# Optimization experiments

Hardware: AMD Instinct MI355X
Metric: run time of the kernel (lower is better)

## Reference

```python
import jax, jax.numpy as jnp
import numpy as np

N_NODES = 50000
N_EDGES = 800000
IN_CH = 128
HID = 64
OUT_CH = 2
N_GRAPHS = 512


def gcn_conv(x, edge_index, W, b, num_nodes):
    # PyG GCNConv: h = x @ W, add self-loops, sym-normalize, scatter-add, add bias
    loop = jnp.arange(num_nodes, dtype=edge_index.dtype)
    src = jnp.concatenate([edge_index[0], loop])
    dst = jnp.concatenate([edge_index[1], loop])
    deg = jax.ops.segment_sum(jnp.ones_like(dst, dtype=x.dtype), dst, num_segments=num_nodes)
    dinv = jnp.where(deg > 0, jax.lax.rsqrt(deg), 0.0)
    norm = dinv[src] * dinv[dst]                      # [E+N]
    h = x @ W                                         # [N, HID]
    msg = h[src] * norm[:, None]                      # gather + scale
    out = jax.ops.segment_sum(msg, dst, num_segments=num_nodes)  # scatter-add
    return out + b


def global_mean_pool(x, batch, num_graphs):
    s = jax.ops.segment_sum(x, batch, num_segments=num_graphs)
    cnt = jax.ops.segment_sum(jnp.ones((x.shape[0],), x.dtype), batch, num_segments=num_graphs)
    return s / jnp.maximum(cnt, 1.0)[:, None]


def setup_inputs() -> dict:
    key = jax.random.key(0)
    ks = jax.random.split(key, 9)
    x = jax.random.normal(ks[0], (N_NODES, IN_CH), dtype=jnp.float32)
    edge_index = jax.random.randint(ks[1], (2, N_EDGES), 0, N_NODES, dtype=jnp.int64)
    batch = jnp.sort(jax.random.randint(ks[2], (N_NODES,), 0, N_GRAPHS, dtype=jnp.int64))
    W1 = jax.random.normal(ks[3], (IN_CH, HID), dtype=jnp.float32) * (1.0 / np.sqrt(IN_CH))
    b1 = jnp.zeros((HID,), dtype=jnp.float32)
    W2 = jax.random.normal(ks[4], (HID, HID), dtype=jnp.float32) * (1.0 / np.sqrt(HID))
    b2 = jnp.zeros((HID,), dtype=jnp.float32)
    Wl = jax.random.normal(ks[5], (HID, OUT_CH), dtype=jnp.float32) * (1.0 / np.sqrt(HID))
    bl = jnp.zeros((OUT_CH,), dtype=jnp.float32)
    return {"x": x, "edge_index": edge_index, "batch": batch,
            "W1": W1, "b1": b1, "W2": W2, "b2": b2, "Wl": Wl, "bl": bl}


def reference(x, edge_index, batch, W1, b1, W2, b2, Wl, bl):
    h = jax.nn.relu(gcn_conv(x, edge_index, W1, b1, N_NODES))
    h = jax.nn.relu(gcn_conv(h, edge_index, W2, b2, N_NODES))
    g = global_mean_pool(h, batch, N_GRAPHS)          # [N_GRAPHS, HID]
    return g @ Wl + bl                                # [N_GRAPHS, OUT_CH]
```

## Files before the change

### kernel.cpp

```cpp
#include <hip/hip_runtime.h>

constexpr int HID = 64;
constexpr int RB = 128;
constexpr int KC = 32;
constexpr int NPB = 128;
constexpr int MAXBUCK = 512;
constexpr int CAP = 2560;
constexpr int CHUNK = 4096;

__global__ __launch_bounds__(256) void k_bucket(const int* __restrict__ src,
                                                const int* __restrict__ dst, int nE,
                                                int* __restrict__ bcursor,
                                                int2* __restrict__ pairs, int nBuck) {
  __shared__ int hist[MAXBUCK];
  __shared__ int base[MAXBUCK];
  const int t = threadIdx.x;
  const int e0 = blockIdx.x * CHUNK;
  const int eEnd = min(e0 + CHUNK, nE);
  for (int i = t; i < nBuck; i += 256) hist[i] = 0;
  __syncthreads();
  for (int e = e0 + t; e < eEnd; e += 256)
    atomicAdd(&hist[dst[e] >> 7], 1);
  __syncthreads();
  for (int i = t; i < nBuck; i += 256) {
    int c = hist[i];
    int r = (c > 0) ? atomicAdd(&bcursor[i], c) : 0;
    base[i] = i * CAP + r;
    hist[i] = 0;
  }
  __syncthreads();
  for (int e = e0 + t; e < eEnd; e += 256) {
    int d = dst[e];
    int b = d >> 7;
    int idx = atomicAdd(&hist[b], 1);
    pairs[base[b] + idx] = make_int2(src[e], d);
  }
}

__global__ __launch_bounds__(256) void k_place(const int2* __restrict__ pairs,
                                               const int* __restrict__ bcursor,
                                               int* __restrict__ csr,
                                               int* __restrict__ row_lo,
                                               int* __restrict__ row_hi,
                                               float* __restrict__ dinv, int nN) {
  __shared__ int cnt[NPB], sc[NPB], cur[NPB];
  const int t = threadIdx.x;
  const int b = blockIdx.x;
  const int vbase = b * NPB;
  const int lo = b * CAP;
  const int npairs = bcursor[b];
  if (t < NPB) cnt[t] = 0;
  __syncthreads();
  for (int p = t; p < npairs; p += 256)
    atomicAdd(&cnt[pairs[lo + p].y - vbase], 1);
  __syncthreads();
  if (t < NPB) sc[t] = cnt[t];
  __syncthreads();
  for (int d = 1; d < NPB; d <<= 1) {
    int x = 0;
    if (t < NPB) { x = sc[t]; if (t >= d) x += sc[t - d]; }
    __syncthreads();
    if (t < NPB) sc[t] = x;
    __syncthreads();
  }
  if (t < NPB && vbase + t < nN) {
    int ex = sc[t] - cnt[t];
    row_lo[vbase + t] = lo + ex;
    row_hi[vbase + t] = lo + sc[t];
    dinv[vbase + t] = rsqrtf((float)cnt[t] + 1.0f);
    cur[t] = lo + ex;
  }
  __syncthreads();
  for (int p = t; p < npairs; p += 256) {
    int2 e = pairs[lo + p];
    int pos = atomicAdd(&cur[e.y - vbase], 1);
    csr[pos] = e.x;
  }
}

template <int K>
__global__ __launch_bounds__(256) void k_mm_tile(const float* __restrict__ X,
                                                 const float* __restrict__ W,
                                                 const float* __restrict__ dinv,
                                                 float* __restrict__ out, int nRows) {
  __shared__ float Xs[RB][KC + 1];
  __shared__ float Ws[KC][HID];

  const int t    = threadIdx.x;
  const int lane = t & 63;
  const int wid  = t >> 6;
  const int rg   = lane >> 3;
  const int cg   = lane & 7;
  const int rb   = blockIdx.x * RB;
  const int rloc = wid * 32 + rg * 4;

  float acc[4][8];
#pragma unroll
  for (int i = 0; i < 4; ++i)
#pragma unroll
    for (int j = 0; j < 8; ++j) acc[i][j] = 0.f;

  for (int c = 0; c < K / KC; ++c) {
    const int k0 = c * KC;
    {
      const int r  = t >> 1;
      const int kh = (t & 1) * 16;
      const int grow = rb + r;
      if (grow < nRows) {
        const float* p = X + (size_t)grow * K + k0 + kh;
#pragma unroll
        for (int q = 0; q < 4; ++q) {
          const float4 v = *(const float4*)(p + q * 4);
          float* d = &Xs[r][kh + q * 4];
          d[0] = v.x; d[1] = v.y; d[2] = v.z; d[3] = v.w;
        }
      }
    }
    {
      const float* p = W + (size_t)(k0 + (t >> 3)) * HID + (t & 7) * 8;
      const float4 v0 = *(const float4*)p;
      const float4 v1 = *(const float4*)(p + 4);
      float* d = &Ws[t >> 3][(t & 7) * 8];
      ((float4*)d)[0] = v0;
      ((float4*)d)[1] = v1;
    }
    __syncthreads();

#pragma unroll
    for (int k = 0; k < KC; ++k) {
      const float4 w0 = *(const float4*)&Ws[k][cg * 8];
      const float4 w1 = *(const float4*)&Ws[k][cg * 8 + 4];
      float xv[4];
#pragma unroll
      for (int i = 0; i < 4; ++i) xv[i] = Xs[rloc + i][k];
#pragma unroll
      for (int i = 0; i < 4; ++i) {
        acc[i][0] = fmaf(xv[i], w0.x, acc[i][0]);
        acc[i][1] = fmaf(xv[i], w0.y, acc[i][1]);
        acc[i][2] = fmaf(xv[i], w0.z, acc[i][2]);
        acc[i][3] = fmaf(xv[i], w0.w, acc[i][3]);
        acc[i][4] = fmaf(xv[i], w1.x, acc[i][4]);
        acc[i][5] = fmaf(xv[i], w1.y, acc[i][5]);
        acc[i][6] = fmaf(xv[i], w1.z, acc[i][6]);
        acc[i][7] = fmaf(xv[i], w1.w, acc[i][7]);
      }
    }
    __syncthreads();
  }

#pragma unroll
  for (int i = 0; i < 4; ++i) {
    const int row = rb + rloc + i;
    if (row < nRows) {
      const float s = dinv[row];
      float4 o0, o1;
      o0.x = acc[i][0] * s; o0.y = acc[i][1] * s; o0.z = acc[i][2] * s; o0.w = acc[i][3] * s;
      o1.x = acc[i][4] * s; o1.y = acc[i][5] * s; o1.z = acc[i][6] * s; o1.w = acc[i][7] * s;
      float* p = out + (size_t)row * HID + cg * 8;
      ((float4*)p)[0] = o0;
      ((float4*)p)[1] = o1;
    }
  }
}

__global__ __launch_bounds__(256) void k_gather4(const int* __restrict__ csr,
                                                 const int* __restrict__ row_lo,
                                                 const int* __restrict__ row_hi,
                                                 const float4* __restrict__ H4,
                                                 const float* __restrict__ dinv,
                                                 const float* __restrict__ b,
                                                 float4* __restrict__ out4, int nN) {
  const int t = threadIdx.x;
  const int wid = t >> 6;
  const int lane = t & 63;
  const int ng = lane >> 4;
  const int cq = lane & 15;
  const int v = blockIdx.x * 16 + wid * 4 + ng;
  const int vv = min(v, nN - 1);
  const int lo = row_lo[vv];
  const int cnt = row_hi[vv] - lo;

  double acc[4][4];
#pragma unroll
  for (int c = 0; c < 4; ++c)
#pragma unroll
    for (int q = 0; q < 4; ++q) acc[c][q] = 0.0;
  {
    const float4 sv = H4[(size_t)vv * 16 + cq];
    acc[0][0] = (double)sv.x; acc[0][1] = (double)sv.y;
    acc[0][2] = (double)sv.z; acc[0][3] = (double)sv.w;
  }

  for (int base = 0; base < cnt; base += 16) {
    int idxv = (base + cq < cnt) ? csr[lo + base + cq] : 0;
#pragma unroll
    for (int j = 0; j < 16; ++j) {
      int s = __shfl(idxv, (ng << 4) + j, 64);
      if (base + j < cnt) {
        const float4 h = H4[(size_t)s * 16 + cq];
        acc[j & 3][0] += (double)h.x;
        acc[j & 3][1] += (double)h.y;
        acc[j & 3][2] += (double)h.z;
        acc[j & 3][3] += (double)h.w;
      }
    }
  }

  if (v < nN) {
    const float dv = dinv[v];
    const float4 bb = ((const float4*)b)[cq];
    float4 o;
    o.x = fmaxf(fmaf(dv, (float)((acc[0][0] + acc[1][0]) + (acc[2][0] + acc[3][0])), bb.x), 0.f);
    o.y = fmaxf(fmaf(dv, (float)((acc[0][1] + acc[1][1]) + (acc[2][1] + acc[3][1])), bb.y), 0.f);
    o.z = fmaxf(fmaf(dv, (float)((acc[0][2] + acc[1][2]) + (acc[2][2] + acc[3][2])), bb.z), 0.f);
    o.w = fmaxf(fmaf(dv, (float)((acc[0][3] + acc[1][3]) + (acc[2][3] + acc[3][3])), bb.w), 0.f);
    out4[(size_t)v * 16 + cq] = o;
  }
}

__device__ inline int lowerb(const int* __restrict__ a, int n, int key) {
  int lo = 0, hi = n;
  while (lo < hi) {
    int mid = (lo + hi) >> 1;
    if (a[mid] < key) lo = mid + 1; else hi = mid;
  }
  return lo;
}

__global__ __launch_bounds__(256) void k_pool_head(const float* __restrict__ Z,
                                                   const int* __restrict__ batch, int nN,
                                                   const float* __restrict__ Wl,
                                                   const float* __restrict__ bl,
                                                   float* __restrict__ out) {
  int g = blockIdx.x;
  int lane = threadIdx.x & 63;
  int wid = threadIdx.x >> 6;
  int lo = lowerb(batch, nN, g);
  int hi = lowerb(batch, nN, g + 1);
  double acc = 0.0;
  for (int r = lo + wid; r < hi; r += 4) acc += (double)Z[(size_t)r * HID + lane];
  __shared__ double s[4][HID];
  s[wid][lane] = acc;
  __syncthreads();
  if (wid == 0) {
    double tot = (s[0][lane] + s[1][lane]) + (s[2][lane] + s[3][lane]);
    double mean = tot / (double)max(hi - lo, 1);
    double p0 = mean * (double)Wl[lane * 2 + 0];
    double p1 = mean * (double)Wl[lane * 2 + 1];
#pragma unroll
    for (int off = 32; off; off >>= 1) {
      p0 += __shfl_xor(p0, off, 64);
      p1 += __shfl_xor(p1, off, 64);
    }
    if (lane == 0) {
      out[g * 2 + 0] = (float)(p0 + (double)bl[0]);
      out[g * 2 + 1] = (float)(p1 + (double)bl[1]);
    }
  }
}

extern "C" void kernel_launch(void* const* d_in, const int* in_sizes, int n_in,
                              void* d_out, int out_size, void* d_ws, size_t ws_size,
                              hipStream_t stream) {
  const float* x     = (const float*)d_in[0];
  const int*   ei    = (const int*)d_in[1];
  const int*   batch = (const int*)d_in[2];
  const float* W1    = (const float*)d_in[3];
  const float* b1    = (const float*)d_in[4];
  const float* W2    = (const float*)d_in[5];
  const float* b2    = (const float*)d_in[6];
  const float* Wl    = (const float*)d_in[7];
  const float* bl    = (const float*)d_in[8];
  float* out = (float*)d_out;

  const int nN = in_sizes[2];
  const int nE = in_sizes[1] / 2;
  const int nG = out_size / 2;
  const int* src = ei;
  const int* dst = ei + nE;

  char* ws = (char*)d_ws;
  size_t off = 0;
  auto alloc = [&](size_t bytes) {
    char* p = ws + off;
    off += (bytes + 255) & ~(size_t)255;
    return p;
  };
  int*   bcursor = (int*)alloc(MAXBUCK * 4);
  int*   row_lo  = (int*)alloc((size_t)nN * 4);
  int*   row_hi  = (int*)alloc((size_t)nN * 4);
  int*   csr     = (int*)alloc((size_t)MAXBUCK * CAP * 4);
  float* dinv    = (float*)alloc((size_t)nN * 4);
  float* A       = (float*)alloc((size_t)nN * HID * 4);
  float* B       = (float*)alloc((size_t)nN * HID * 4);
  int2*  pairs   = (int2*)A;

  const int nBuck = (nN + NPB - 1) / NPB;

  hipMemsetAsync(bcursor, 0, MAXBUCK * 4, stream);
  k_bucket<<<(nE + CHUNK - 1) / CHUNK, 256, 0, stream>>>(src, dst, nE, bcursor, pairs, nBuck);
  k_place<<<nBuck, 256, 0, stream>>>(pairs, bcursor, csr, row_lo, row_hi, dinv, nN);

  k_mm_tile<128><<<(nN + RB - 1) / RB, 256, 0, stream>>>(x, W1, dinv, A, nN);
  k_gather4<<<(nN + 15) / 16, 256, 0, stream>>>(csr, row_lo, row_hi, (const float4*)A,
                                                dinv, b1, (float4*)B, nN);

  k_mm_tile<64><<<(nN + RB - 1) / RB, 256, 0, stream>>>(B, W2, dinv, A, nN);
  k_gather4<<<(nN + 15) / 16, 256, 0, stream>>>(csr, row_lo, row_hi, (const float4*)A,
                                                dinv, b2, (float4*)B, nN);

  k_pool_head<<<nG, 256, 0, stream>>>(B, batch, nN, Wl, bl, out);
}
```

Before: 149.9 us.

## Fuse layer-1 gather with layer-2 matmul into one kernel

```diff
diff --git a/kernel.cpp b/kernel.cpp
--- a/kernel.cpp
+++ b/kernel.cpp
@@ -6,7 +6,7 @@
 constexpr int NPB = 128;
 constexpr int MAXBUCK = 512;
 constexpr int CAP = 2560;
-constexpr int CHUNK = 4096;
+constexpr int CHUNK = 2048;
 
 __global__ __launch_bounds__(256) void k_bucket(const int* __restrict__ src,
                                                 const int* __restrict__ dst, int nE,
@@ -160,6 +160,89 @@
       ((float4*)p)[0] = o0;
       ((float4*)p)[1] = o1;
     }
+  }
+}
+
+__global__ __launch_bounds__(256) void k_gather_mm(const int* __restrict__ csr,
+                                                   const int* __restrict__ row_lo,
+                                                   const int* __restrict__ row_hi,
+                                                   const float4* __restrict__ H4,
+                                                   const float* __restrict__ dinv,
+                                                   const float* __restrict__ b,
+                                                   const float* __restrict__ W2,
+                                                   float4* __restrict__ out4, int nN) {
+  __shared__ float W2s[HID][HID];
+  __shared__ float z1s[16][68];
+
+  const int t = threadIdx.x;
+  for (int i = t; i < HID * HID / 4; i += 256)
+    ((float4*)W2s)[i] = ((const float4*)W2)[i];
+  __syncthreads();
+
+  const int wid = t >> 6;
+  const int lane = t & 63;
+  const int ng = lane >> 4;
+  const int cq = lane & 15;
+  const int nl = wid * 4 + ng;
+  const int v = blockIdx.x * 16 + nl;
+  const int vv = min(v, nN - 1);
+  const int lo = row_lo[vv];
+  const int cnt = row_hi[vv] - lo;
+
+  double acc[4][4];
+#pragma unroll
+  for (int c = 0; c < 4; ++c)
+#pragma unroll
+    for (int q = 0; q < 4; ++q) acc[c][q] = 0.0;
+  {
+    const float4 sv = H4[(size_t)vv * 16 + cq];
+    acc[0][0] = (double)sv.x; acc[0][1] = (double)sv.y;
+    acc[0][2] = (double)sv.z; acc[0][3] = (double)sv.w;
+  }
+
+  for (int base = 0; base < cnt; base += 16) {
+    int idxv = (base + cq < cnt) ? csr[lo + base + cq] : 0;
+#pragma unroll
+    for (int j = 0; j < 16; ++j) {
+      int s = __shfl(idxv, (ng << 4) + j, 64);
+      if (base + j < cnt) {
+        const float4 h = H4[(size_t)s * 16 + cq];
+        acc[j & 3][0] += (double)h.x;
+        acc[j & 3][1] += (double)h.y;
+        acc[j & 3][2] += (double)h.z;
+        acc[j & 3][3] += (double)h.w;
+      }
+    }
+  }
+
+  {
+    const float dv = dinv[vv];
+    const float4 bb = ((const float4*)b)[cq];
+    float4 z;
+    z.x = fmaxf(fmaf(dv, (float)((acc[0][0] + acc[1][0]) + (acc[2][0] + acc[3][0])), bb.x), 0.f);
+    z.y = fmaxf(fmaf(dv, (float)((acc[0][1] + acc[1][1]) + (acc[2][1] + acc[3][1])), bb.y), 0.f);
+    z.z = fmaxf(fmaf(dv, (float)((acc[0][2] + acc[1][2]) + (acc[2][2] + acc[3][2])), bb.z), 0.f);
+    z.w = fmaxf(fmaf(dv, (float)((acc[0][3] + acc[1][3]) + (acc[2][3] + acc[3][3])), bb.w), 0.f);
+    float* zp = &z1s[nl][cq * 4];
+    zp[0] = z.x; zp[1] = z.y; zp[2] = z.z; zp[3] = z.w;
+  }
+
+  float h0 = 0.f, h1 = 0.f, h2 = 0.f, h3 = 0.f;
+#pragma unroll 8
+  for (int k = 0; k < HID; ++k) {
+    const float zk = z1s[nl][k];
+    const float4 w = *(const float4*)&W2s[k][cq * 4];
+    h0 = fmaf(zk, w.x, h0);
+    h1 = fmaf(zk, w.y, h1);
+    h2 = fmaf(zk, w.z, h2);
+    h3 = fmaf(zk, w.w, h3);
+  }
+
+  if (v < nN) {
+    const float dv = dinv[v];
+    float4 o;
+    o.x = h0 * dv; o.y = h1 * dv; o.z = h2 * dv; o.w = h3 * dv;
+    out4[(size_t)v * 16 + cq] = o;
   }
 }
 
@@ -302,12 +385,12 @@
   k_place<<<nBuck, 256, 0, stream>>>(pairs, bcursor, csr, row_lo, row_hi, dinv, nN);
 
   k_mm_tile<128><<<(nN + RB - 1) / RB, 256, 0, stream>>>(x, W1, dinv, A, nN);
-  k_gather4<<<(nN + 15) / 16, 256, 0, stream>>>(csr, row_lo, row_hi, (const float4*)A,
-                                                dinv, b1, (float4*)B, nN);
-
-  k_mm_tile<64><<<(nN + RB - 1) / RB, 256, 0, stream>>>(B, W2, dinv, A, nN);
-  k_gather4<<<(nN + 15) / 16, 256, 0, stream>>>(csr, row_lo, row_hi, (const float4*)A,
-                                                dinv, b2, (float4*)B, nN);
-
-  k_pool_head<<<nG, 256, 0, stream>>>(B, batch, nN, Wl, bl, out);
-}
+
+  k_gather_mm<<<(nN + 15) / 16, 256, 0, stream>>>(csr, row_lo, row_hi, (const float4*)A,
+                                                  dinv, b1, W2, (float4*)B, nN);
+
+  k_gather4<<<(nN + 15) / 16, 256, 0, stream>>>(csr, row_lo, row_hi, (const float4*)B,
+                                                dinv, b2, (float4*)A, nN);
+
+  k_pool_head<<<nG, 256, 0, stream>>>(A, batch, nN, Wl, bl, out);
+}
```

Measured after the change: 140.1 us. -6.6%, faster.
